# Kernel tuning notes

Measured on AMD Instinct MI355X. Metric: run time of the kernel, lower is better.

Reference implementation:

```python
import jax, jax.numpy as jnp
import numpy as np

RADIUS = 0.1
MAX_NEIGHBORS = 64


def setup_inputs() -> dict:
    key0 = jax.random.key(0)
    k1, k2 = jax.random.split(key0)
    query = jax.random.uniform(k1, (4, 2048, 3), dtype=jnp.float32)
    key = jax.random.uniform(k2, (4, 8192, 3), dtype=jnp.float32)
    return {"query": query, "key": key}


def reference(query, key):
    # PointNet++-style ball query: for each query point, the indices of the
    # first MAX_NEIGHBORS key points (in key order) with squared distance
    # < RADIUS^2; remaining slots are padded with the first found neighbor
    # index (0 if no neighbor exists, matching zero-initialized CUDA output).
    B, N1, _ = query.shape
    N2 = key.shape[1]
    K = MAX_NEIGHBORS

    # [B, N1, N2] squared pairwise distances
    d2 = jnp.sum((query[:, :, None, :] - key[:, None, :, :]) ** 2, axis=-1)
    within = d2 < jnp.float32(RADIUS) ** 2  # [B, N1, N2] bool

    # slot each valid neighbor lands in (in key-index order)
    pos = jnp.cumsum(within.astype(jnp.int32), axis=-1) - 1  # [B, N1, N2]
    take = within & (pos < K)
    slot = jnp.where(take, pos, K)  # invalid entries routed to dummy slot K

    n2_idx = jnp.broadcast_to(jnp.arange(N2, dtype=jnp.int32), (B, N1, N2))
    b_idx = jnp.arange(B)[:, None, None]
    n1_idx = jnp.arange(N1)[None, :, None]

    out = jnp.full((B, N1, K + 1), -1, dtype=jnp.int32)
    # slots < K are unique per (b, n1); duplicates only at dummy slot K
    out = out.at[b_idx, n1_idx, slot].set(n2_idx)
    out = out[..., :K]  # drop dummy slot

    # pad empty slots with index of first in-radius neighbor (0 if none)
    first = jnp.argmax(within, axis=-1).astype(jnp.int32)  # [B, N1]
    out = jnp.where(out < 0, first[..., None], out)
    return out
```

## Files before the change

### kernel.cpp

```cpp
#include <hip/hip_runtime.h>


constexpr int   K    = 64;
constexpr float R2   = 0.01f;
constexpr int   B    = 4;
constexpr int   N1   = 2048;
constexpr int   N2   = 8192;
constexpr int   GC   = 5;
constexpr int   NCELL = GC * GC * GC;
constexpr float INVCELL = 5.0f;
constexpr int   BLOCKS  = 256;
constexpr int   THREADS = 1024;
constexpr int   WAVES   = 16;
constexpr int   QPB     = (B * N1) / BLOCKS;
constexpr int   QPW     = QPB / WAVES;
constexpr int   PER     = N2 / THREADS;

__device__ __forceinline__ int cell_of(float v) {
    int c = (int)(v * INVCELL);
    return c < 0 ? 0 : (c > GC - 1 ? GC - 1 : c);
}

__global__ __launch_bounds__(1024) void ballquery_fused_kernel(
    const float* __restrict__ query,
    const float* __restrict__ key,
    int* __restrict__ out)
{
    __shared__ float4 skey[N2];
    __shared__ int    hist[NCELL];
    __shared__ int    sbuf[128];
    __shared__ int    start[NCELL + 1];
    __shared__ unsigned int bm[WAVES * 256];

    const int blk  = blockIdx.x;
    const int b    = blk >> 6;
    const int t    = threadIdx.x;
    const int lane = t & 63;
    const int wv   = t >> 6;

    if (t < NCELL) hist[t] = 0;
    __syncthreads();

    const float* kb = key + (size_t)b * N2 * 3;
    float kx[PER], ky[PER], kz[PER];
    int   kc[PER];
    #pragma unroll
    for (int r = 0; r < PER; ++r) {
        const int i = r * THREADS + t;
        kx[r] = kb[i * 3 + 0];
        ky[r] = kb[i * 3 + 1];
        kz[r] = kb[i * 3 + 2];
        kc[r] = (cell_of(kx[r]) * GC + cell_of(ky[r])) * GC + cell_of(kz[r]);
        atomicAdd(&hist[kc[r]], 1);
    }
    __syncthreads();

    if (t < 128) sbuf[t] = (t < NCELL) ? hist[t] : 0;
    __syncthreads();
    for (int off = 1; off < 128; off <<= 1) {
        int v = 0;
        if (t < 128 && t >= off) v = sbuf[t - off];
        __syncthreads();
        if (t < 128) sbuf[t] += v;
        __syncthreads();
    }
    if (t < NCELL) start[t + 1] = sbuf[t];
    if (t == 0)    start[0] = 0;
    __syncthreads();
    if (t < NCELL) hist[t] = start[t];
    __syncthreads();

    #pragma unroll
    for (int r = 0; r < PER; ++r) {
        const int i = r * THREADS + t;
        const int pos = atomicAdd(&hist[kc[r]], 1);
        float4 v;
        v.x = kx[r]; v.y = ky[r]; v.z = kz[r];
        v.w = __int_as_float(i);
        skey[pos] = v;
    }
    __syncthreads();

    unsigned int* wbm = bm + wv * 256;
    const int qbase = blk * QPB + wv * QPW;

    #pragma unroll
    for (int qi = 0; qi < QPW; ++qi) {
        const int q = qbase + qi;

        const float qx = query[q * 3 + 0];
        const float qy = query[q * 3 + 1];
        const float qz = query[q * 3 + 2];

        const float ux = qx * INVCELL, uy = qy * INVCELL, uz = qz * INVCELL;
        const int cx = cell_of(qx), cy = cell_of(qy), cz = cell_of(qz);
        const int nx = (ux - cx < 0.5f) ? cx - 1 : cx + 1;
        const int ny = (uy - cy < 0.5f) ? cy - 1 : cy + 1;
        const int nz = (uz - cz < 0.5f) ? cz - 1 : cz + 1;
        const int xlo = max(0, min(cx, nx)), xhi = min(GC - 1, max(cx, nx));
        const int ylo = max(0, min(cy, ny)), yhi = min(GC - 1, max(cy, ny));
        const int zlo = max(0, min(cz, nz)), zhi = min(GC - 1, max(cz, nz));

        uint4 zz; zz.x = zz.y = zz.z = zz.w = 0u;
        ((uint4*)wbm)[lane] = zz;
        __threadfence_block();

        for (int xx = xlo; xx <= xhi; ++xx) {
            for (int yy = ylo; yy <= yhi; ++yy) {
                const int colz = (xx * GC + yy) * GC;
                const int s = start[colz + zlo];
                const int e = start[colz + zhi + 1];
                for (int t0 = s; t0 < e; t0 += 64) {
                    const int i = t0 + lane;
                    const float4 kv = skey[min(i, e - 1)];
                    const float dx = kv.x - qx;
                    const float dy = kv.y - qy;
                    const float dz = kv.z - qz;
                    const bool within = (i < e) &&
                        (dx * dx + dy * dy + dz * dz < R2);
                    if (within) {
                        const int id = __float_as_int(kv.w);
                        atomicOr(&wbm[id >> 5], 1u << (id & 31));
                    }
                }
            }
        }
        __threadfence_block();

        const uint4 w = ((const uint4*)wbm)[lane];
        const int c = __popc(w.x) + __popc(w.y) + __popc(w.z) + __popc(w.w);

        int x = c;
        #pragma unroll
        for (int off = 1; off < 64; off <<= 1) {
            int y = __shfl_up(x, off);
            if (lane >= off) x += y;
        }
        const int base = x - c;
        const int cnt  = __shfl(x, 63);

        int fs;
        if      (w.x) fs = __builtin_ctz(w.x);
        else if (w.y) fs = 32 + __builtin_ctz(w.y);
        else if (w.z) fs = 64 + __builtin_ctz(w.z);
        else if (w.w) fs = 96 + __builtin_ctz(w.w);
        else          fs = 0;
        int myfirst = c ? (lane << 7) + fs : 0x7fffffff;
        #pragma unroll
        for (int off = 32; off; off >>= 1)
            myfirst = min(myfirst, __shfl_xor(myfirst, off));
        const int firstIdx = (cnt == 0) ? 0 : myfirst;

        int* op = out + q * K;
        int slot = base;
        unsigned int wr[4] = {w.x, w.y, w.z, w.w};
        #pragma unroll
        for (int r = 0; r < 4; ++r) {
            unsigned int m = wr[r];
            const int bb = (lane << 7) + (r << 5);
            while (m) {
                const int bp = __builtin_ctz(m);
                m &= m - 1;
                if (slot < K) op[slot] = bb + bp;
                ++slot;
            }
        }

        const int kpad = cnt < K ? cnt : K;
        const int s2 = kpad + lane;
        if (s2 < K) op[s2] = firstIdx;
    }
}

extern "C" void kernel_launch(void* const* d_in, const int* in_sizes, int n_in,
                              void* d_out, int out_size, void* d_ws, size_t ws_size,
                              hipStream_t stream) {
    const float* query = (const float*)d_in[0];
    const float* key   = (const float*)d_in[1];
    int* out = (int*)d_out;

    ballquery_fused_kernel<<<BLOCKS, THREADS, 0, stream>>>(query, key, out);
}
```

Measured before the change: 68.76 us.

## Replace cell sort with ballot-built per-column key bitmaps and register hit masks

Drops the histogram/scan/scatter counting sort of keys into 3D cells and instead stores keys SoA in shared memory and builds, per 2D (x,y) column, a 64-bit-per-word occupancy bitmap using wave ballots. Each lane owns 128 consecutive key indices and walks candidate bits to test distances, accumulating hits in registers instead of atomicOr into a shared bitmap. This removes setup atomics and many barriers but loses z-culling and introduces per-lane serial, divergent loops.

```diff
diff --git a/kernel.cpp b/kernel.cpp
--- a/kernel.cpp
+++ b/kernel.cpp
@@ -7,30 +7,40 @@
 constexpr int   N1   = 2048;
 constexpr int   N2   = 8192;
 constexpr int   GC   = 5;
-constexpr int   NCELL = GC * GC * GC;
 constexpr float INVCELL = 5.0f;
+constexpr int   NCOL    = GC * GC;
+constexpr int   NWORD   = N2 / 64;
+constexpr int   WSTRIDE = NWORD + 2;
 constexpr int   BLOCKS  = 256;
 constexpr int   THREADS = 1024;
 constexpr int   WAVES   = 16;
 constexpr int   QPB     = (B * N1) / BLOCKS;
 constexpr int   QPW     = QPB / WAVES;
-constexpr int   PER     = N2 / THREADS;
 
 __device__ __forceinline__ int cell_of(float v) {
     int c = (int)(v * INVCELL);
     return c < 0 ? 0 : (c > GC - 1 ? GC - 1 : c);
 }
 
-__global__ __launch_bounds__(1024) void ballquery_fused_kernel(
+__device__ __forceinline__ unsigned long long sel5(
+    unsigned long long a0, unsigned long long a1, unsigned long long a2,
+    unsigned long long a3, unsigned long long a4, int s)
+{
+    unsigned long long r = a0;
+    r = (s == 1) ? a1 : r;
+    r = (s == 2) ? a2 : r;
+    r = (s == 3) ? a3 : r;
+    r = (s == 4) ? a4 : r;
+    return r;
+}
+
+__global__ __launch_bounds__(1024) void ballquery_fused2_kernel(
     const float* __restrict__ query,
     const float* __restrict__ key,
     int* __restrict__ out)
 {
-    __shared__ float4 skey[N2];
-    __shared__ int    hist[NCELL];
-    __shared__ int    sbuf[128];
-    __shared__ int    start[NCELL + 1];
-    __shared__ unsigned int bm[WAVES * 256];
+    __shared__ float kx[N2], ky[N2], kz[N2];
+    __shared__ unsigned long long colbm[NCOL * WSTRIDE];
 
     const int blk  = blockIdx.x;
     const int b    = blk >> 6;
@@ -38,53 +48,43 @@
     const int lane = t & 63;
     const int wv   = t >> 6;
 
-    if (t < NCELL) hist[t] = 0;
-    __syncthreads();
+    const float* kb = key + (size_t)b * N2 * 3;
+    const int cdiv = lane / 5;
+    const int cmod = lane - cdiv * 5;
 
-    const float* kb = key + (size_t)b * N2 * 3;
-    float kx[PER], ky[PER], kz[PER];
-    int   kc[PER];
     #pragma unroll
-    for (int r = 0; r < PER; ++r) {
-        const int i = r * THREADS + t;
-        kx[r] = kb[i * 3 + 0];
-        ky[r] = kb[i * 3 + 1];
-        kz[r] = kb[i * 3 + 2];
-        kc[r] = (cell_of(kx[r]) * GC + cell_of(ky[r])) * GC + cell_of(kz[r]);
-        atomicAdd(&hist[kc[r]], 1);
+    for (int r = 0; r < NWORD / WAVES; ++r) {
+        const int word = r * WAVES + wv;
+        const int i = (word << 6) + lane;
+        const float x = kb[i * 3 + 0];
+        const float y = kb[i * 3 + 1];
+        const float z = kb[i * 3 + 2];
+        kx[i] = x; ky[i] = y; kz[i] = z;
+
+        const int cx = cell_of(x);
+        const int cy = cell_of(y);
+        const unsigned long long bx0 = __ballot(cx == 0);
+        const unsigned long long bx1 = __ballot(cx == 1);
+        const unsigned long long bx2 = __ballot(cx == 2);
+        const unsigned long long bx3 = __ballot(cx == 3);
+        const unsigned long long bx4 = __ballot(cx == 4);
+        const unsigned long long by0 = __ballot(cy == 0);
+        const unsigned long long by1 = __ballot(cy == 1);
+        const unsigned long long by2 = __ballot(cy == 2);
+        const unsigned long long by3 = __ballot(cy == 3);
+        const unsigned long long by4 = __ballot(cy == 4);
+
+        if (lane < NCOL) {
+            const unsigned long long m =
+                sel5(bx0, bx1, bx2, bx3, bx4, cdiv) &
+                sel5(by0, by1, by2, by3, by4, cmod);
+            colbm[lane * WSTRIDE + word] = m;
+        }
     }
     __syncthreads();
 
-    if (t < 128) sbuf[t] = (t < NCELL) ? hist[t] : 0;
-    __syncthreads();
-    for (int off = 1; off < 128; off <<= 1) {
-        int v = 0;
-        if (t < 128 && t >= off) v = sbuf[t - off];
-        __syncthreads();
-        if (t < 128) sbuf[t] += v;
-        __syncthreads();
-    }
-    if (t < NCELL) start[t + 1] = sbuf[t];
-    if (t == 0)    start[0] = 0;
-    __syncthreads();
-    if (t < NCELL) hist[t] = start[t];
-    __syncthreads();
-
-    #pragma unroll
-    for (int r = 0; r < PER; ++r) {
-        const int i = r * THREADS + t;
-        const int pos = atomicAdd(&hist[kc[r]], 1);
-        float4 v;
-        v.x = kx[r]; v.y = ky[r]; v.z = kz[r];
-        v.w = __int_as_float(i);
-        skey[pos] = v;
-    }
-    __syncthreads();
-
-    unsigned int* wbm = bm + wv * 256;
     const int qbase = blk * QPB + wv * QPW;
 
-    #pragma unroll
     for (int qi = 0; qi < QPW; ++qi) {
         const int q = qbase + qi;
 
@@ -92,60 +92,64 @@
         const float qy = query[q * 3 + 1];
         const float qz = query[q * 3 + 2];
 
-        const float ux = qx * INVCELL, uy = qy * INVCELL, uz = qz * INVCELL;
-        const int cx = cell_of(qx), cy = cell_of(qy), cz = cell_of(qz);
+        const float ux = qx * INVCELL, uy = qy * INVCELL;
+        const int cx = cell_of(qx), cy = cell_of(qy);
         const int nx = (ux - cx < 0.5f) ? cx - 1 : cx + 1;
         const int ny = (uy - cy < 0.5f) ? cy - 1 : cy + 1;
-        const int nz = (uz - cz < 0.5f) ? cz - 1 : cz + 1;
         const int xlo = max(0, min(cx, nx)), xhi = min(GC - 1, max(cx, nx));
         const int ylo = max(0, min(cy, ny)), yhi = min(GC - 1, max(cy, ny));
-        const int zlo = max(0, min(cz, nz)), zhi = min(GC - 1, max(cz, nz));
 
-        uint4 zz; zz.x = zz.y = zz.z = zz.w = 0u;
-        ((uint4*)wbm)[lane] = zz;
-        __threadfence_block();
+        const int w0 = lane << 1;
+        const int ibase = lane << 7;
+        unsigned long long hit0 = 0ull, hit1 = 0ull;
 
         for (int xx = xlo; xx <= xhi; ++xx) {
             for (int yy = ylo; yy <= yhi; ++yy) {
-                const int colz = (xx * GC + yy) * GC;
-                const int s = start[colz + zlo];
-                const int e = start[colz + zhi + 1];
-                for (int t0 = s; t0 < e; t0 += 64) {
-                    const int i = t0 + lane;
-                    const float4 kv = skey[min(i, e - 1)];
-                    const float dx = kv.x - qx;
-                    const float dy = kv.y - qy;
-                    const float dz = kv.z - qz;
-                    const bool within = (i < e) &&
-                        (dx * dx + dy * dy + dz * dz < R2);
-                    if (within) {
-                        const int id = __float_as_int(kv.w);
-                        atomicOr(&wbm[id >> 5], 1u << (id & 31));
-                    }
+                const int c = xx * GC + yy;
+                const unsigned long long cand0 = colbm[c * WSTRIDE + w0];
+                const unsigned long long cand1 = colbm[c * WSTRIDE + w0 + 1];
+
+                unsigned long long m = cand0;
+                while (m) {
+                    const int bp = __builtin_ctzll(m);
+                    m &= m - 1;
+                    const int i = ibase + bp;
+                    const float dx = kx[i] - qx;
+                    const float dy = ky[i] - qy;
+                    const float dz = kz[i] - qz;
+                    if (dx * dx + dy * dy + dz * dz < R2)
+                        hit0 |= 1ull << bp;
+                }
+                m = cand1;
+                while (m) {
+                    const int bp = __builtin_ctzll(m);
+                    m &= m - 1;
+                    const int i = ibase + 64 + bp;
+                    const float dx = kx[i] - qx;
+                    const float dy = ky[i] - qy;
+                    const float dz = kz[i] - qz;
+                    if (dx * dx + dy * dy + dz * dz < R2)
+                        hit1 |= 1ull << bp;
                 }
             }
         }
-        __threadfence_block();
 
-        const uint4 w = ((const uint4*)wbm)[lane];
-        const int c = __popc(w.x) + __popc(w.y) + __popc(w.z) + __popc(w.w);
+        const int c0 = __popcll(hit0) + __popcll(hit1);
 
-        int x = c;
+        int x = c0;
         #pragma unroll
         for (int off = 1; off < 64; off <<= 1) {
             int y = __shfl_up(x, off);
             if (lane >= off) x += y;
         }
-        const int base = x - c;
+        const int base = x - c0;
         const int cnt  = __shfl(x, 63);
 
         int fs;
-        if      (w.x) fs = __builtin_ctz(w.x);
-        else if (w.y) fs = 32 + __builtin_ctz(w.y);
-        else if (w.z) fs = 64 + __builtin_ctz(w.z);
-        else if (w.w) fs = 96 + __builtin_ctz(w.w);
-        else          fs = 0;
-        int myfirst = c ? (lane << 7) + fs : 0x7fffffff;
+        if      (hit0) fs = __builtin_ctzll(hit0);
+        else if (hit1) fs = 64 + __builtin_ctzll(hit1);
+        else           fs = 0;
+        int myfirst = c0 ? ibase + fs : 0x7fffffff;
         #pragma unroll
         for (int off = 32; off; off >>= 1)
             myfirst = min(myfirst, __shfl_xor(myfirst, off));
@@ -153,17 +157,19 @@
 
         int* op = out + q * K;
         int slot = base;
-        unsigned int wr[4] = {w.x, w.y, w.z, w.w};
-        #pragma unroll
-        for (int r = 0; r < 4; ++r) {
-            unsigned int m = wr[r];
-            const int bb = (lane << 7) + (r << 5);
-            while (m) {
-                const int bp = __builtin_ctz(m);
-                m &= m - 1;
-                if (slot < K) op[slot] = bb + bp;
-                ++slot;
-            }
+        unsigned long long m = hit0;
+        while (m) {
+            const int bp = __builtin_ctzll(m);
+            m &= m - 1;
+            if (slot < K) op[slot] = ibase + bp;
+            ++slot;
+        }
+        m = hit1;
+        while (m) {
+            const int bp = __builtin_ctzll(m);
+            m &= m - 1;
+            if (slot < K) op[slot] = ibase + 64 + bp;
+            ++slot;
         }
 
         const int kpad = cnt < K ? cnt : K;
@@ -179,5 +185,5 @@
     const float* key   = (const float*)d_in[1];
     int* out = (int*)d_out;
 
-    ballquery_fused_kernel<<<BLOCKS, THREADS, 0, stream>>>(query, key, out);
+    ballquery_fused2_kernel<<<BLOCKS, THREADS, 0, stream>>>(query, key, out);
 }
```

New measurement: 80.49 us. +17.1%, slower.
